# Performance work log

Measured on AMD Instinct MI355X. Metric: run time of the kernel, lower is better.

Reference implementation:

```python
import jax, jax.numpy as jnp
import numpy as np

D = 1024
H = 16
DH = D // H
F = 4096
B, S = 4, 2048
EPS = 1e-5


def _ln(x, g, b):
    m = jnp.mean(x, axis=-1, keepdims=True)
    v = jnp.var(x, axis=-1, keepdims=True)
    return (x - m) * jax.lax.rsqrt(v + EPS) * g + b


def setup_inputs() -> dict:
    key = jax.random.key(0)
    ks = jax.random.split(key, 16)
    s = 0.02
    return {
        "x": jax.random.normal(ks[0], (B, S, D), jnp.float32),
        "key_padding_mask": jnp.zeros((B, S), jnp.bool_),
        "Wq": jax.random.normal(ks[1], (D, D), jnp.float32) * s,
        "bq": jnp.zeros((D,), jnp.float32),
        "Wk": jax.random.normal(ks[2], (D, D), jnp.float32) * s,
        "bk": jnp.zeros((D,), jnp.float32),
        "Wv": jax.random.normal(ks[3], (D, D), jnp.float32) * s,
        "bv": jnp.zeros((D,), jnp.float32),
        "Wo": jax.random.normal(ks[4], (D, D), jnp.float32) * s,
        "bo": jnp.zeros((D,), jnp.float32),
        "W1": jax.random.normal(ks[5], (F, D), jnp.float32) * s,
        "b1": jnp.zeros((F,), jnp.float32),
        "W2": jax.random.normal(ks[6], (D, F), jnp.float32) * s,
        "b2": jnp.zeros((D,), jnp.float32),
        "ln1_g": jnp.ones((D,), jnp.float32),
        "ln1_b": jnp.zeros((D,), jnp.float32),
        "ln2_g": jnp.ones((D,), jnp.float32),
        "ln2_b": jnp.zeros((D,), jnp.float32),
    }


def _attn(x, kpm, Wq, bq, Wk, bk, Wv, bv, Wo, bo):
    b, s, d = x.shape
    scaling = DH ** (-0.5)
    q = (x @ Wq.T + bq) * scaling
    k = x @ Wk.T + bk
    v = x @ Wv.T + bv
    q = q.reshape(b, s, H, DH)
    k = k.reshape(b, s, H, DH)
    v = v.reshape(b, s, H, DH)
    # [b,h,q,k]
    scores = jnp.einsum("bqhd,bkhd->bhqk", q, k)
    scores = jnp.where(kpm[:, None, None, :], -jnp.inf, scores)
    p = jax.nn.softmax(scores.astype(jnp.float32), axis=-1).astype(q.dtype)
    out = jnp.einsum("bhqk,bkhd->bqhd", p, v).reshape(b, s, d)
    return out @ Wo.T + bo


def reference(x, key_padding_mask, Wq, bq, Wk, bk, Wv, bv, Wo, bo,
              W1, b1, W2, b2, ln1_g, ln1_b, ln2_g, ln2_b):
    # post-LN (normalize_before=False), dropout in eval mode (identity)
    x = _ln(x + _attn(x, key_padding_mask, Wq, bq, Wk, bk, Wv, bv, Wo, bo), ln1_g, ln1_b)
    h = jax.nn.gelu(x @ W1.T + b1, approximate=False)
    x = _ln(x + (h @ W2.T + b2), ln2_g, ln2_b)
    return x
```

## Files before the change

### kernel.cpp

```cpp
#include <hip/hip_runtime.h>
#include <hip/hip_bf16.h>
#include <math.h>

typedef short bf16x8 __attribute__((ext_vector_type(8)));
typedef float f32x4 __attribute__((ext_vector_type(4)));
typedef float f32x2 __attribute__((ext_vector_type(2)));

__device__ __forceinline__ unsigned short f2bfu(float f) {
    __hip_bfloat16 h = __float2bfloat16(f);
    return __builtin_bit_cast(unsigned short, h);
}

__device__ __forceinline__ float fexp2(float x) {
    float r;
    asm("v_exp_f32 %0, %1" : "=v"(r) : "v"(x));
    return r;
}

__device__ __forceinline__ unsigned cvtpk_bf16(float lo, float hi) {
    unsigned r;
    asm("v_cvt_pk_bf16_f32 %0, %1, %2" : "=v"(r) : "v"(lo), "v"(hi));
    return r;
}

__device__ __forceinline__ float max3f(float a, float b, float c) {
    float r;
    asm("v_max3_f32 %0, %1, %2, %3" : "=v"(r) : "v"(a), "v"(b), "v"(c));
    return r;
}

__device__ __forceinline__ f32x2 pk_sub2(f32x2 a, f32x2 b) {
    f32x2 r;
    asm("v_pk_add_f32 %0, %1, %2 neg_lo:[0,1] neg_hi:[0,1]" : "=v"(r) : "v"(a), "v"(b));
    return r;
}

__device__ __forceinline__ f32x2 pk_add2(f32x2 a, f32x2 b) {
    f32x2 r;
    asm("v_pk_add_f32 %0, %1, %2" : "=v"(r) : "v"(a), "v"(b));
    return r;
}

__device__ __forceinline__ float gelu_fast(float x) {
    const float x2 = x * x;
    const float z = x * (0.7978845608f + 0.0356774081f * x2);
    const float e = fexp2(z * 2.88539008f);
    const float r = __builtin_amdgcn_rcpf(e + 1.0f);
    return x * (1.0f - r);
}

__device__ __forceinline__ void gload_lds16(const void* gsrc, void* ldst) {
    __builtin_amdgcn_global_load_lds((const __attribute__((address_space(1))) void*)gsrc,
                                     (__attribute__((address_space(3))) void*)ldst,
                                     16, 0, 0);
}

#define MFMA __builtin_amdgcn_mfma_f32_16x16x32_bf16
#define SBAR __builtin_amdgcn_s_barrier
#define SCHB __builtin_amdgcn_sched_barrier

__global__ __launch_bounds__(256)
void cvt_all_kernel(const float4* __restrict__ x,  ushort4* __restrict__ xb,
                    const float4* __restrict__ wq, ushort4* __restrict__ wqb,
                    const float4* __restrict__ wk, ushort4* __restrict__ wkb,
                    const float4* __restrict__ wv, ushort4* __restrict__ wvb,
                    const float4* __restrict__ wo, ushort4* __restrict__ wob,
                    const float4* __restrict__ w1, ushort4* __restrict__ w1b,
                    const float4* __restrict__ w2, ushort4* __restrict__ w2b)
{
    const int i = blockIdx.x * 256 + threadIdx.x;
    const float4* src;
    ushort4* dst;
    int base;
    if (i < 2097152)      { src = x;  dst = xb;  base = 0; }
    else if (i < 2359296) { src = wq; dst = wqb; base = 2097152; }
    else if (i < 2621440) { src = wk; dst = wkb; base = 2359296; }
    else if (i < 2883584) { src = wv; dst = wvb; base = 2621440; }
    else if (i < 3145728) { src = wo; dst = wob; base = 2883584; }
    else if (i < 4194304) { src = w1; dst = w1b; base = 3145728; }
    else                  { src = w2; dst = w2b; base = 4194304; }
    const float4 v = src[i - base];
    ushort4 o;
    o.x = f2bfu(v.x); o.y = f2bfu(v.y); o.z = f2bfu(v.z); o.w = f2bfu(v.w);
    dst[i - base] = o;
}

enum { EPI_QKV = 0, EPI_RES_OB = 2, EPI_GELU = 3 };

template<int EPI>
__global__ __launch_bounds__(512, 1)
void gemm8p(const __hip_bfloat16* __restrict__ A,
            const __hip_bfloat16* __restrict__ W,
            const float* __restrict__ bias,
            const void* __restrict__ resv,
            void* __restrict__ outp,
            int M, int N, int K)
{
    __shared__ __hip_bfloat16 As[2][256 * 64];
    __shared__ __hip_bfloat16 Bs[2][256 * 64];
    const int tid = threadIdx.x;
    const int lane = tid & 63;
    const int wid = tid >> 6;
    const int wr = wid >> 1;
    const int wc = wid & 1;
    const int g = lane >> 4, lr = lane & 15;
    const int row0 = blockIdx.x * 256;
    const int col0 = blockIdx.y * 256;

    f32x4 acc[4][8];
    const f32x4 zero = {0.f, 0.f, 0.f, 0.f};
#pragma unroll
    for (int m = 0; m < 4; ++m)
#pragma unroll
        for (int n = 0; n < 8; ++n) acc[m][n] = zero;

    const int arl = tid >> 3;
    const int agc = (tid & 7) ^ (arl & 7);
    const __hip_bfloat16* Abase = A + (size_t)(row0 + arl) * K + agc * 8;
    const __hip_bfloat16* Bbase = W + (size_t)(col0 + arl) * K + agc * 8;

    auto stageA = [&](int bi, int kt) {
#pragma unroll
        for (int q = 0; q < 4; ++q)
            gload_lds16(Abase + (size_t)(q * 64) * K + kt * 64,
                        (char*)As[bi] + q * 8192 + tid * 16);
    };
    auto stageB = [&](int bi, int h, int kt) {
#pragma unroll
        for (int j = 0; j < 2; ++j)
            gload_lds16(Bbase + (size_t)(h * 128 + j * 64) * K + kt * 64,
                        (char*)Bs[bi] + h * 16384 + j * 8192 + tid * 16);
    };

    const int NT = K >> 6;
    stageA(0, 0);
    stageB(0, 0, 0);
    stageB(0, 1, 0);
    stageA(1, 1);
    asm volatile("s_waitcnt vmcnt(4)" ::: "memory");
    SBAR();
    SCHB(0);

    const int swz = lr & 7;
    const int arow = wr * 64;
    const int brow = wc * 128;

    for (int t = 0; t < NT; ++t) {
        const int bi = t & 1;
        const __hip_bfloat16* Ab = As[bi];
        const __hip_bfloat16* Bb = Bs[bi];
        bf16x8 a[4], b0[4], b1[4];

#pragma unroll
        for (int m = 0; m < 4; ++m)
            a[m] = *(const bf16x8*)(Ab + (arow + m * 16 + lr) * 64 + ((g ^ swz) * 8));
#pragma unroll
        for (int n = 0; n < 4; ++n)
            b0[n] = *(const bf16x8*)(Bb + (brow + n * 16 + lr) * 64 + ((g ^ swz) * 8));
        if (t + 1 < NT) stageB(bi ^ 1, 0, t + 1);
        SCHB(0);
        SBAR();
        __builtin_amdgcn_s_setprio(1);
#pragma unroll
        for (int m = 0; m < 4; ++m)
#pragma unroll
            for (int n = 0; n < 4; ++n)
                acc[m][n] = MFMA(a[m], b0[n], acc[m][n], 0, 0, 0);
        __builtin_amdgcn_s_setprio(0);
        SBAR();

#pragma unroll
        for (int n = 0; n < 4; ++n)
            b1[n] = *(const bf16x8*)(Bb + (brow + (n + 4) * 16 + lr) * 64 + ((g ^ swz) * 8));
        if (t + 1 < NT) stageB(bi ^ 1, 1, t + 1);
        SCHB(0);
        SBAR();
        __builtin_amdgcn_s_setprio(1);
#pragma unroll
        for (int m = 0; m < 4; ++m)
#pragma unroll
            for (int n = 0; n < 4; ++n)
                acc[m][n + 4] = MFMA(a[m], b1[n], acc[m][n + 4], 0, 0, 0);
        __builtin_amdgcn_s_setprio(0);
        SBAR();

#pragma unroll
        for (int m = 0; m < 4; ++m)
            a[m] = *(const bf16x8*)(Ab + (arow + m * 16 + lr) * 64 + (((4 + g) ^ swz) * 8));
#pragma unroll
        for (int n = 0; n < 4; ++n)
            b0[n] = *(const bf16x8*)(Bb + (brow + n * 16 + lr) * 64 + (((4 + g) ^ swz) * 8));
        SCHB(0);
        SBAR();
        __builtin_amdgcn_s_setprio(1);
#pragma unroll
        for (int m = 0; m < 4; ++m)
#pragma unroll
            for (int n = 0; n < 4; ++n)
                acc[m][n] = MFMA(a[m], b0[n], acc[m][n], 0, 0, 0);
        __builtin_amdgcn_s_setprio(0);
        SBAR();

#pragma unroll
        for (int n = 0; n < 4; ++n)
            b1[n] = *(const bf16x8*)(Bb + (brow + (n + 4) * 16 + lr) * 64 + (((4 + g) ^ swz) * 8));
        if (t + 2 < NT) stageA(bi, t + 2);
        SCHB(0);
        SBAR();
        __builtin_amdgcn_s_setprio(1);
#pragma unroll
        for (int m = 0; m < 4; ++m)
#pragma unroll
            for (int n = 0; n < 4; ++n)
                acc[m][n + 4] = MFMA(a[m], b1[n], acc[m][n + 4], 0, 0, 0);
        __builtin_amdgcn_s_setprio(0);
        if (t + 1 < NT) {
            if (t + 2 < NT) asm volatile("s_waitcnt vmcnt(4)" ::: "memory");
            else            asm volatile("s_waitcnt vmcnt(0)" ::: "memory");
            SBAR();
            SCHB(0);
        }
    }

#pragma unroll
    for (int n = 0; n < 8; ++n) {
        const int cc = col0 + wc * 128 + n * 16 + lr;
        const float bv = bias[cc];
#pragma unroll
        for (int m = 0; m < 4; ++m) {
            const int rbase = row0 + wr * 64 + m * 16 + g * 4;
#pragma unroll
            for (int r = 0; r < 4; ++r) {
                const size_t idx = (size_t)(rbase + r) * N + cc;
                float v = acc[m][n][r] + bv;
                if (EPI == EPI_RES_OB) {
                    const float rv = __bfloat162float(((const __hip_bfloat16*)resv)[idx]);
                    ((__hip_bfloat16*)outp)[idx] = __float2bfloat16(v + rv);
                } else if (EPI == EPI_GELU) {
                    ((__hip_bfloat16*)outp)[idx] = __float2bfloat16(gelu_fast(v));
                }
            }
        }
    }
}

template<int EPI>
__global__ __launch_bounds__(256, 3)
void gemm_bt(const __hip_bfloat16* __restrict__ A,
             const __hip_bfloat16* __restrict__ W,
             const float* __restrict__ bias,
             const void* __restrict__ resv,
             float scale,
             void* __restrict__ outp, void* __restrict__ outp2, void* __restrict__ outp3,
             int M, int N, int K)
{
    __shared__ __hip_bfloat16 As[3][128 * 32];
    __shared__ __hip_bfloat16 Ws[3][128 * 32];
    const int tid = threadIdx.x;
    const int lane = tid & 63;
    const int wid = tid >> 6;
    const int wr = wid >> 1, wc = wid & 1;
    const int g = lane >> 4, lr = lane & 15;
    const int row0 = blockIdx.x * 128;
    const int col0 = blockIdx.y * 128;

    f32x4 acc[4][4];
    const f32x4 zero = {0.f, 0.f, 0.f, 0.f};
#pragma unroll
    for (int m = 0; m < 4; ++m)
#pragma unroll
        for (int n = 0; n < 4; ++n) acc[m][n] = zero;

    const int c0 = tid, c1 = tid + 256;
    const int ar0 = c0 >> 2, ac0 = (c0 & 3) * 8;
    const int ar1 = c1 >> 2, ac1 = (c1 & 3) * 8;
    const __hip_bfloat16* Arow0 = A + (size_t)(row0 + ar0) * K + ac0;
    const __hip_bfloat16* Arow1 = A + (size_t)(row0 + ar1) * K + ac1;
    const __hip_bfloat16* Wrow0 = W + (size_t)(col0 + ar0) * K + ac0;
    const __hip_bfloat16* Wrow1 = W + (size_t)(col0 + ar1) * K + ac1;

    auto stage = [&](int bi, int k0) {
        gload_lds16(Arow0 + k0, (char*)As[bi] + c0 * 16);
        gload_lds16(Arow1 + k0, (char*)As[bi] + c1 * 16);
        gload_lds16(Wrow0 + k0, (char*)Ws[bi] + c0 * 16);
        gload_lds16(Wrow1 + k0, (char*)Ws[bi] + c1 * 16);
    };

    const int NT = K >> 5;
    stage(0, 0);
    stage(1, 32);
    asm volatile("s_waitcnt vmcnt(4)" ::: "memory");
    SBAR();
    SCHB(0);

    int cur = 0, stg = 2;
    int kpre = 64;
    for (int t = 0; t < NT; ++t) {
        if (t + 2 < NT) stage(stg, kpre);

        bf16x8 af[4], wf[4];
#pragma unroll
        for (int m = 0; m < 4; ++m)
            af[m] = *(const bf16x8*)(As[cur] + (wr * 64 + m * 16 + lr) * 32 + g * 8);
#pragma unroll
        for (int n = 0; n < 4; ++n)
            wf[n] = *(const bf16x8*)(Ws[cur] + (wc * 64 + n * 16 + lr) * 32 + g * 8);
#pragma unroll
        for (int m = 0; m < 4; ++m)
#pragma unroll
            for (int n = 0; n < 4; ++n)
                acc[m][n] = MFMA(af[m], wf[n], acc[m][n], 0, 0, 0);

        if (t + 1 < NT) {
            if (t + 2 < NT) asm volatile("s_waitcnt vmcnt(4)" ::: "memory");
            else            asm volatile("s_waitcnt vmcnt(0)" ::: "memory");
            SBAR();
            SCHB(0);
        }
        cur = (cur == 2) ? 0 : cur + 1;
        stg = (stg == 2) ? 0 : stg + 1;
        kpre += 32;
    }

#pragma unroll
    for (int n = 0; n < 4; ++n) {
        const int cc = col0 + wc * 64 + n * 16 + lr;
        const float bv = bias[cc];
#pragma unroll
        for (int m = 0; m < 4; ++m) {
            const int rbase = row0 + wr * 64 + m * 16 + g * 4;
            if (EPI == EPI_QKV) {
                const int seg = col0 >> 10;
                if (seg == 2) {
                    ushort4 u;
                    u.x = f2bfu(acc[m][n][0] + bv);
                    u.y = f2bfu(acc[m][n][1] + bv);
                    u.z = f2bfu(acc[m][n][2] + bv);
                    u.w = f2bfu(acc[m][n][3] + bv);
                    const int cc2 = cc - 2048;
                    const int h_ = cc2 >> 6, dh = cc2 & 63;
                    const int bb = rbase >> 11;
                    const int s = rbase & 2047;
                    *(ushort4*)((__hip_bfloat16*)outp3 +
                                (((size_t)bb * 16 + h_) * 64 + dh) * 2048 + s) = u;
                } else {
                    const float sc = (seg == 0) ? scale : 1.0f;
                    __hip_bfloat16* dst = (seg == 0) ? (__hip_bfloat16*)outp
                                                     : (__hip_bfloat16*)outp2;
                    const int ccl = cc & 1023;
#pragma unroll
                    for (int r = 0; r < 4; ++r)
                        dst[(size_t)(rbase + r) * 1024 + ccl] =
                            __float2bfloat16((acc[m][n][r] + bv) * sc);
                }
            } else {
#pragma unroll
                for (int r = 0; r < 4; ++r) {
                    const size_t idx = (size_t)(rbase + r) * N + cc;
                    float v = acc[m][n][r] + bv;
                    if (EPI == EPI_RES_OB) {
                        const float rv = __bfloat162float(((const __hip_bfloat16*)resv)[idx]);
                        ((__hip_bfloat16*)outp)[idx] = __float2bfloat16(v + rv);
                    } else if (EPI == EPI_GELU) {
                        ((__hip_bfloat16*)outp)[idx] = __float2bfloat16(gelu_fast(v));
                    }
                }
            }
        }
    }
}

__global__ __launch_bounds__(512, 4)
void attn_flash3(const __hip_bfloat16* __restrict__ Q,
                 const __hip_bfloat16* __restrict__ K,
                 const __hip_bfloat16* __restrict__ VT,
                 const unsigned char* __restrict__ kpm,
                 __hip_bfloat16* __restrict__ O)
{
    __shared__ __hip_bfloat16 Ks[2][64 * 64];
    __shared__ __hip_bfloat16 VTs[2][64 * 64];
    __shared__ __hip_bfloat16 Plds[8][32 * 64];

    const int tid = threadIdx.x;
    const int lane = tid & 63;
    const int w = tid >> 6;
    const int g = lane >> 4, lr = lane & 15;

    const int orig = blockIdx.y * 8 + blockIdx.x;
    const int nl = (orig & 7) * 64 + (orig >> 3);
    const int qb = nl & 7;
    const int bh = nl >> 3;

    const int b = bh >> 4, h = bh & 15;
    const int q0 = qb * 256 + w * 32;
    const size_t tokbase = (size_t)b * 2048;
    const __hip_bfloat16* VTbh = VT + (size_t)bh * 64 * 2048;

    unsigned tmask = 0;
#pragma unroll
    for (int i = 0; i < 8; ++i) {
        const unsigned mv = *(const unsigned*)(kpm + tokbase + i * 256 + lane * 4);
        const unsigned long long bal = __ballot((int)(mv != 0u));
#pragma unroll
        for (int j = 0; j < 4; ++j)
            if ((bal >> (16 * j)) & 0xFFFFull) tmask |= (1u << (i * 4 + j));
    }

    bf16x8 qf[2][2];
#pragma unroll
    for (int qn = 0; qn < 2; ++qn)
#pragma unroll
        for (int f = 0; f < 2; ++f)
            qf[qn][f] = *(const bf16x8*)(Q + (tokbase + q0 + qn * 16 + lr) * 1024 +
                                         h * 64 + f * 32 + g * 8);

    f32x4 o[2][4];
    const f32x4 zero = {0.f, 0.f, 0.f, 0.f};
#pragma unroll
    for (int qa = 0; qa < 2; ++qa)
#pragma unroll
        for (int nd = 0; nd < 4; ++nd) o[qa][nd] = zero;
    float m_run[2], l_part[2];
#pragma unroll
    for (int qn = 0; qn < 2; ++qn) { m_run[qn] = -1e30f; l_part[qn] = 0.f; }

    __hip_bfloat16* Pw = Plds[w];

    const int srow = w * 8 + (lane >> 3);
    const int sblk = (lane & 7) ^ (srow & 7);
    const __hip_bfloat16* Ksrc = K + (tokbase + srow) * 1024 + h * 64 + sblk * 8;
    const __hip_bfloat16* Vsrc = VTbh + (size_t)srow * 2048 + sblk * 8;

    auto stage = [&](int bufi, int kv0) {
        gload_lds16(Ksrc + (size_t)kv0 * 1024, (char*)&Ks[bufi][w * 512] + lane * 16);
        gload_lds16(Vsrc + kv0, (char*)&VTs[bufi][w * 512] + lane * 16);
    };

    stage(0, 0);
    __syncthreads();
    int buf = 0;

    for (int t = 0; t < 32; ++t) {
        const int kv0 = t * 64;
        if (t < 31) stage(buf ^ 1, kv0 + 64);

        f32x4 st[4][2];
        __builtin_amdgcn_s_setprio(1);
#pragma unroll
        for (int km = 0; km < 4; ++km) {
            bf16x8 kf[2];
#pragma unroll
            for (int f = 0; f < 2; ++f)
                kf[f] = *(const bf16x8*)(&Ks[buf][(km * 16 + lr) * 64 +
                                                  (((f * 4 + g) ^ (lr & 7)) * 8)]);
#pragma unroll
            for (int qn = 0; qn < 2; ++qn) {
                st[km][qn] = MFMA(kf[0], qf[qn][0], zero, 0, 0, 0);
                st[km][qn] = MFMA(kf[1], qf[qn][1], st[km][qn], 0, 0, 0);
            }
        }
        __builtin_amdgcn_s_setprio(0);

        if (tmask & (1u << t)) {
            const float NEG = -1e30f;
#pragma unroll
            for (int km = 0; km < 4; ++km) {
                const unsigned mu = *(const unsigned*)(kpm + tokbase + kv0 + km * 16 + g * 4);
#pragma unroll
                for (int r = 0; r < 4; ++r) {
                    if ((mu >> (8 * r)) & 0xFFu) {
#pragma unroll
                        for (int qn = 0; qn < 2; ++qn) st[km][qn][r] = NEG;
                    }
                }
            }
        }

        float pm[2];
#pragma unroll
        for (int qn = 0; qn < 2; ++qn) {
            const float v1 = max3f(st[0][qn][0], st[0][qn][1], st[0][qn][2]);
            const float v2 = max3f(st[0][qn][3], st[1][qn][0], st[1][qn][1]);
            const float v3 = max3f(st[1][qn][2], st[1][qn][3], st[2][qn][0]);
            const float v4 = max3f(st[2][qn][1], st[2][qn][2], st[2][qn][3]);
            const float v5 = max3f(st[3][qn][0], st[3][qn][1], st[3][qn][2]);
            pm[qn] = fmaxf(max3f(v1, v2, v3), max3f(v4, v5, st[3][qn][3]));
        }
        const int trig = (pm[0] > m_run[0] + 8.f) | (pm[1] > m_run[1] + 8.f);
        if (__any(trig)) {
            float alpha_q[2];
#pragma unroll
            for (int qn = 0; qn < 2; ++qn) {
                float rm = pm[qn];
                rm = fmaxf(rm, __shfl_xor(rm, 16));
                rm = fmaxf(rm, __shfl_xor(rm, 32));
                const float mnew = fmaxf(m_run[qn], rm);
                const float al = fexp2(m_run[qn] - mnew);
                l_part[qn] *= al;
                m_run[qn] = mnew;
                alpha_q[qn] = al;
            }
#pragma unroll
            for (int qa = 0; qa < 2; ++qa)
#pragma unroll
                for (int r = 0; r < 4; ++r) {
                    const float av = __shfl(alpha_q[qa], g * 4 + r, 16);
#pragma unroll
                    for (int nd = 0; nd < 4; ++nd) o[qa][nd][r] *= av;
                }
        }

#pragma unroll
        for (int qn = 0; qn < 2; ++qn) {
            const float mm = m_run[qn];
            const f32x2 mm2 = {mm, mm};
            f32x2 lacc = {0.f, 0.f};
#pragma unroll
            for (int km = 0; km < 4; ++km) {
                const f32x2 s01 = {st[km][qn][0], st[km][qn][1]};
                const f32x2 s23 = {st[km][qn][2], st[km][qn][3]};
                const f32x2 d01 = pk_sub2(s01, mm2);
                const f32x2 d23 = pk_sub2(s23, mm2);
                f32x2 p01, p23;
                p01.x = fexp2(d01.x);
                p01.y = fexp2(d01.y);
                p23.x = fexp2(d23.x);
                p23.y = fexp2(d23.y);
                lacc = pk_add2(lacc, pk_add2(p01, p23));
                uint2 pk;
                pk.x = cvtpk_bf16(p01.x, p01.y);
                pk.y = cvtpk_bf16(p23.x, p23.y);
                const int cs = (km * 2 + (g >> 1)) ^ (lr & 7);
                *(uint2*)(Pw + (qn * 16 + lr) * 64 + cs * 8 + (g & 1) * 4) = pk;
            }
            l_part[qn] += lacc.x + lacc.y;
        }

        __builtin_amdgcn_s_setprio(1);
#pragma unroll
        for (int f = 0; f < 2; ++f) {
            bf16x8 pa[2];
#pragma unroll
            for (int qa = 0; qa < 2; ++qa)
                pa[qa] = *(const bf16x8*)(Pw + (qa * 16 + lr) * 64 +
                                          (((f * 4 + g) ^ (lr & 7)) * 8));
#pragma unroll
            for (int nd = 0; nd < 4; ++nd) {
                bf16x8 vb = *(const bf16x8*)(&VTs[buf][(nd * 16 + lr) * 64 +
                                                       (((f * 4 + g) ^ (lr & 7)) * 8)]);
#pragma unroll
                for (int qa = 0; qa < 2; ++qa)
                    o[qa][nd] = MFMA(pa[qa], vb, o[qa][nd], 0, 0, 0);
            }
        }
        __builtin_amdgcn_s_setprio(0);

        __syncthreads();
        buf ^= 1;
    }

    float linv[2];
#pragma unroll
    for (int qn = 0; qn < 2; ++qn) {
        float lt = l_part[qn];
        lt += __shfl_xor(lt, 16);
        lt += __shfl_xor(lt, 32);
        linv[qn] = 1.0f / lt;
    }
#pragma unroll
    for (int qa = 0; qa < 2; ++qa)
#pragma unroll
        for (int r = 0; r < 4; ++r) {
            const float lv = __shfl(linv[qa], g * 4 + r, 16);
            const size_t row = tokbase + q0 + qa * 16 + g * 4 + r;
#pragma unroll
            for (int nd = 0; nd < 4; ++nd)
                O[row * 1024 + h * 64 + nd * 16 + lr] = __float2bfloat16(o[qa][nd][r] * lv);
        }
}

__global__ __launch_bounds__(256)
void ln_b_kernel(const __hip_bfloat16* __restrict__ in, const float* __restrict__ gamma,
                 const float* __restrict__ beta, float* __restrict__ outf,
                 __hip_bfloat16* __restrict__ outb)
{
    const int row = blockIdx.x;
    const int tid = threadIdx.x;
    const ushort4 u = ((const ushort4*)(in + (size_t)row * 1024))[tid];
    float v0 = __bfloat162float(__builtin_bit_cast(__hip_bfloat16, u.x));
    float v1 = __bfloat162float(__builtin_bit_cast(__hip_bfloat16, u.y));
    float v2 = __bfloat162float(__builtin_bit_cast(__hip_bfloat16, u.z));
    float v3 = __bfloat162float(__builtin_bit_cast(__hip_bfloat16, u.w));
    float s = (v0 + v1) + (v2 + v3);
    float s2 = (v0 * v0 + v1 * v1) + (v2 * v2 + v3 * v3);
#pragma unroll
    for (int off = 1; off < 64; off <<= 1) {
        s += __shfl_xor(s, off);
        s2 += __shfl_xor(s2, off);
    }
    __shared__ float red[8];
    const int wv = tid >> 6;
    if ((tid & 63) == 0) { red[wv] = s; red[4 + wv] = s2; }
    __syncthreads();
    s = red[0] + red[1] + red[2] + red[3];
    s2 = red[4] + red[5] + red[6] + red[7];
    const float mean = s * (1.f / 1024.f);
    const float var = s2 * (1.f / 1024.f) - mean * mean;
    const float rstd = rsqrtf(var + 1e-5f);
    const float4 gm = ((const float4*)gamma)[tid];
    const float4 bt = ((const float4*)beta)[tid];
    float y0 = (v0 - mean) * rstd * gm.x + bt.x;
    float y1 = (v1 - mean) * rstd * gm.y + bt.y;
    float y2 = (v2 - mean) * rstd * gm.z + bt.z;
    float y3 = (v3 - mean) * rstd * gm.w + bt.w;
    if (outf) {
        float4 y; y.x = y0; y.y = y1; y.z = y2; y.w = y3;
        ((float4*)(outf + (size_t)row * 1024))[tid] = y;
    }
    if (outb) {
        ushort4 ub;
        ub.x = f2bfu(y0); ub.y = f2bfu(y1); ub.z = f2bfu(y2); ub.w = f2bfu(y3);
        ((ushort4*)outb)[row * 256 + tid] = ub;
    }
}

extern "C" void kernel_launch(void* const* d_in, const int* in_sizes, int n_in,
                              void* d_out, int out_size, void* d_ws, size_t ws_size,
                              hipStream_t stream)
{
    const float* x    = (const float*)d_in[0];
    const unsigned char* kpm = (const unsigned char*)d_in[1];
    const float* Wq = (const float*)d_in[2];
    const float* bq = (const float*)d_in[3];
    const float* Wk = (const float*)d_in[4];
    const float* bk = (const float*)d_in[5];
    const float* Wv = (const float*)d_in[6];
    const float* bv = (const float*)d_in[7];
    const float* Wo = (const float*)d_in[8];
    const float* bo = (const float*)d_in[9];
    const float* W1 = (const float*)d_in[10];
    const float* b1 = (const float*)d_in[11];
    const float* W2 = (const float*)d_in[12];
    const float* b2 = (const float*)d_in[13];
    const float* ln1g = (const float*)d_in[14];
    const float* ln1b = (const float*)d_in[15];
    const float* ln2g = (const float*)d_in[16];
    const float* ln2b = (const float*)d_in[17];
    float* out = (float*)d_out;

    char* ws = (char*)d_ws;
    const size_t SZ_ND2 = (size_t)8192 * 1024 * 2;
    size_t off = 0;
    __hip_bfloat16* xb  = (__hip_bfloat16*)(ws + off); off += SZ_ND2;
    __hip_bfloat16* wqb = (__hip_bfloat16*)(ws + off); off += (size_t)1024 * 1024 * 2;
    __hip_bfloat16* wkb = (__hip_bfloat16*)(ws + off); off += (size_t)1024 * 1024 * 2;
    __hip_bfloat16* wvb = (__hip_bfloat16*)(ws + off); off += (size_t)1024 * 1024 * 2;
    __hip_bfloat16* wob = (__hip_bfloat16*)(ws + off); off += (size_t)1024 * 1024 * 2;
    __hip_bfloat16* w1b = (__hip_bfloat16*)(ws + off); off += (size_t)4096 * 1024 * 2;
    __hip_bfloat16* w2b = (__hip_bfloat16*)(ws + off); off += (size_t)4096 * 1024 * 2;
    const size_t qkv0 = off;
    __hip_bfloat16* qbp = (__hip_bfloat16*)(ws + off); off += SZ_ND2;
    __hip_bfloat16* kbp = (__hip_bfloat16*)(ws + off); off += SZ_ND2;
    __hip_bfloat16* vtg = (__hip_bfloat16*)(ws + off); off += SZ_ND2;
    __hip_bfloat16* abp = (__hip_bfloat16*)(ws + off); off += SZ_ND2;
    __hip_bfloat16* hbp = (__hip_bfloat16*)(ws + qkv0);
    __hip_bfloat16* y1b = (__hip_bfloat16*)(ws + off); off += SZ_ND2;
    __hip_bfloat16* x1b = (__hip_bfloat16*)(ws + off); off += SZ_ND2;
    __hip_bfloat16* y2b = y1b;
    float* bqkv = (float*)(ws + off); off += 3072 * 4;

    cvt_all_kernel<<<20480, 256, 0, stream>>>(
        (const float4*)x,  (ushort4*)xb,
        (const float4*)Wq, (ushort4*)wqb,
        (const float4*)Wk, (ushort4*)wkb,
        (const float4*)Wv, (ushort4*)wvb,
        (const float4*)Wo, (ushort4*)wob,
        (const float4*)W1, (ushort4*)w1b,
        (const float4*)W2, (ushort4*)w2b);
    hipMemcpyAsync(bqkv,        bq, 4096, hipMemcpyDeviceToDevice, stream);
    hipMemcpyAsync(bqkv + 1024, bk, 4096, hipMemcpyDeviceToDevice, stream);
    hipMemcpyAsync(bqkv + 2048, bv, 4096, hipMemcpyDeviceToDevice, stream);

    dim3 blk(256);
    const float qscale = 0.125f * 1.44269504088896f;

    gemm_bt<EPI_QKV><<<dim3(64, 24), blk, 0, stream>>>(
        xb, wqb, bqkv, nullptr, qscale, qbp, kbp, vtg, 8192, 3072, 1024);

    attn_flash3<<<dim3(8, 64), 512, 0, stream>>>(qbp, kbp, vtg, kpm, abp);

    gemm_bt<EPI_RES_OB><<<dim3(64, 8), blk, 0, stream>>>(
        abp, wob, bo, xb, 1.0f, y1b, nullptr, nullptr, 8192, 1024, 1024);
    ln_b_kernel<<<8192, 256, 0, stream>>>(y1b, ln1g, ln1b, nullptr, x1b);

    gemm8p<EPI_GELU><<<dim3(32, 16), 512, 0, stream>>>(
        x1b, w1b, b1, nullptr, hbp, 8192, 4096, 1024);
    gemm_bt<EPI_RES_OB><<<dim3(64, 8), blk, 0, stream>>>(
        hbp, w2b, b2, x1b, 1.0f, y2b, nullptr, nullptr, 8192, 1024, 4096);
    ln_b_kernel<<<8192, 256, 0, stream>>>(y2b, ln2g, ln2b, out, nullptr);
}
```

Before: 394.9 us.

## Add 128x256-tile pipelined GEMM kernel for the FFN down-projection

Adds a new 512-thread GEMM kernel with a 128x256 output tile, a triple-buffered A tile and a double-buffered B tile loaded straight into LDS, and split-K-phase staging. The W2 projection (K=4096) now uses it in place of the generic 256-thread gemm_bt. The aim is better operand reuse and better overlap of loads with MFMA work on the long-K GEMM. It also adds an unused scale parameter to gemm8p. The grid is now 256 blocks of 512 threads, which may underfill the device's compute units.

```diff
diff --git a/kernel.cpp b/kernel.cpp
--- a/kernel.cpp
+++ b/kernel.cpp
@@ -93,6 +93,7 @@
             const __hip_bfloat16* __restrict__ W,
             const float* __restrict__ bias,
             const void* __restrict__ resv,
+            float scale,
             void* __restrict__ outp,
             int M, int N, int K)
 {
@@ -225,6 +226,136 @@
 #pragma unroll
     for (int n = 0; n < 8; ++n) {
         const int cc = col0 + wc * 128 + n * 16 + lr;
+        const float bv = bias[cc];
+#pragma unroll
+        for (int m = 0; m < 4; ++m) {
+            const int rbase = row0 + wr * 64 + m * 16 + g * 4;
+#pragma unroll
+            for (int r = 0; r < 4; ++r) {
+                const size_t idx = (size_t)(rbase + r) * N + cc;
+                float v = acc[m][n][r] + bv;
+                if (EPI == EPI_RES_OB) {
+                    const float rv = __bfloat162float(((const __hip_bfloat16*)resv)[idx]);
+                    ((__hip_bfloat16*)outp)[idx] = __float2bfloat16(v + rv);
+                } else if (EPI == EPI_GELU) {
+                    ((__hip_bfloat16*)outp)[idx] = __float2bfloat16(gelu_fast(v));
+                }
+            }
+        }
+    }
+}
+
+template<int EPI>
+__global__ __launch_bounds__(512, 1)
+void gemm2p_w(const __hip_bfloat16* __restrict__ A,
+              const __hip_bfloat16* __restrict__ W,
+              const float* __restrict__ bias,
+              const void* __restrict__ resv,
+              void* __restrict__ outp,
+              int M, int N, int K)
+{
+    __shared__ __hip_bfloat16 As[3][128 * 64];
+    __shared__ __hip_bfloat16 Bs[2][256 * 64];
+    const int tid = threadIdx.x;
+    const int lane = tid & 63;
+    const int wid = tid >> 6;
+    const int wr = wid >> 2;
+    const int wc = wid & 3;
+    const int g = lane >> 4, lr = lane & 15;
+    const int row0 = blockIdx.x * 128;
+    const int col0 = blockIdx.y * 256;
+
+    f32x4 acc[4][4];
+    const f32x4 zero = {0.f, 0.f, 0.f, 0.f};
+#pragma unroll
+    for (int m = 0; m < 4; ++m)
+#pragma unroll
+        for (int n = 0; n < 4; ++n) acc[m][n] = zero;
+
+    const int r0 = tid >> 3;
+    const int gc = (tid & 7) ^ (r0 & 7);
+    const __hip_bfloat16* Abase = A + (size_t)(row0 + r0) * K + gc * 8;
+    const __hip_bfloat16* Bbase = W + (size_t)(col0 + r0) * K + gc * 8;
+
+    auto stageA = [&](int bi, int kt) {
+#pragma unroll
+        for (int j = 0; j < 2; ++j)
+            gload_lds16(Abase + (size_t)(j * 64) * K + kt * 64,
+                        (char*)As[bi] + j * 8192 + tid * 16);
+    };
+    auto stageB = [&](int bi, int kt) {
+#pragma unroll
+        for (int j = 0; j < 4; ++j)
+            gload_lds16(Bbase + (size_t)(j * 64) * K + kt * 64,
+                        (char*)Bs[bi] + j * 8192 + tid * 16);
+    };
+
+    const int NT = K >> 6;
+    stageA(0, 0);
+    stageB(0, 0);
+    stageA(1, 1);
+    asm volatile("s_waitcnt vmcnt(2)" ::: "memory");
+    SBAR();
+    SCHB(0);
+
+    const int swz = lr & 7;
+    const int arow = wr * 64;
+    const int brow = wc * 64;
+    int a_cur = 0;
+
+    for (int t = 0; t < NT; ++t) {
+        const int bu = t & 1;
+        const __hip_bfloat16* Ab = As[a_cur];
+        const __hip_bfloat16* Bb = Bs[bu];
+        const int a_nx2 = (a_cur == 0) ? 2 : a_cur - 1;
+        bf16x8 a[4], b[4];
+
+#pragma unroll
+        for (int m = 0; m < 4; ++m)
+            a[m] = *(const bf16x8*)(Ab + (arow + m * 16 + lr) * 64 + ((g ^ swz) * 8));
+#pragma unroll
+        for (int n = 0; n < 4; ++n)
+            b[n] = *(const bf16x8*)(Bb + (brow + n * 16 + lr) * 64 + ((g ^ swz) * 8));
+        if (t + 1 < NT) stageB(bu ^ 1, t + 1);
+        SCHB(0);
+        SBAR();
+        __builtin_amdgcn_s_setprio(1);
+#pragma unroll
+        for (int m = 0; m < 4; ++m)
+#pragma unroll
+            for (int n = 0; n < 4; ++n)
+                acc[m][n] = MFMA(a[m], b[n], acc[m][n], 0, 0, 0);
+        __builtin_amdgcn_s_setprio(0);
+        SBAR();
+
+#pragma unroll
+        for (int m = 0; m < 4; ++m)
+            a[m] = *(const bf16x8*)(Ab + (arow + m * 16 + lr) * 64 + (((4 + g) ^ swz) * 8));
+#pragma unroll
+        for (int n = 0; n < 4; ++n)
+            b[n] = *(const bf16x8*)(Bb + (brow + n * 16 + lr) * 64 + (((4 + g) ^ swz) * 8));
+        if (t + 2 < NT) stageA(a_nx2, t + 2);
+        SCHB(0);
+        SBAR();
+        __builtin_amdgcn_s_setprio(1);
+#pragma unroll
+        for (int m = 0; m < 4; ++m)
+#pragma unroll
+            for (int n = 0; n < 4; ++n)
+                acc[m][n] = MFMA(a[m], b[n], acc[m][n], 0, 0, 0);
+        __builtin_amdgcn_s_setprio(0);
+        if (t + 1 < NT) {
+            if (t + 2 < NT) asm volatile("s_waitcnt vmcnt(2)" ::: "memory");
+            else            asm volatile("s_waitcnt vmcnt(0)" ::: "memory");
+            SBAR();
+            SCHB(0);
+        }
+        a_cur = (a_cur == 2) ? 0 : a_cur + 1;
+    }
+
+#pragma unroll
+    for (int n = 0; n < 4; ++n) {
+        const int cc = col0 + wc * 64 + n * 16 + lr;
         const float bv = bias[cc];
 #pragma unroll
         for (int m = 0; m < 4; ++m) {
@@ -694,8 +825,8 @@
     ln_b_kernel<<<8192, 256, 0, stream>>>(y1b, ln1g, ln1b, nullptr, x1b);
 
     gemm8p<EPI_GELU><<<dim3(32, 16), 512, 0, stream>>>(
-        x1b, w1b, b1, nullptr, hbp, 8192, 4096, 1024);
-    gemm_bt<EPI_RES_OB><<<dim3(64, 8), blk, 0, stream>>>(
-        hbp, w2b, b2, x1b, 1.0f, y2b, nullptr, nullptr, 8192, 1024, 4096);
+        x1b, w1b, b1, nullptr, 1.0f, hbp, 8192, 4096, 1024);
+    gemm2p_w<EPI_RES_OB><<<dim3(64, 4), 512, 0, stream>>>(
+        hbp, w2b, b2, x1b, y2b, 8192, 1024, 4096);
     ln_b_kernel<<<8192, 256, 0, stream>>>(y2b, ln2g, ln2b, out, nullptr);
 }
```

After: 373.0 us, median of 2. 1.06x faster.
